# Performance work log

Measured on AMD Instinct MI355X. Metric: run time of the kernel, lower is better.

Reference implementation:

```python
import jax, jax.numpy as jnp
import numpy as np

SCALE_REACH = 10.0   # 'scale' in forward
SCALE_COS = 16.0     # CosNorm_Classifier default scale


def setup_inputs() -> dict:
    key = jax.random.key(0)
    ks = jax.random.split(key, 7)
    B, C, F = 64, 1000, 2048
    return {
        "x": jax.random.normal(ks[0], (B, F), jnp.float32),
        "centroids": jax.random.normal(ks[1], (C, F), jnp.float32),
        "W_hall": jax.random.normal(ks[2], (C, F), jnp.float32) * 0.02,
        "b_hall": jax.random.normal(ks[3], (C,), jnp.float32) * 0.02,
        "W_sel": jax.random.normal(ks[4], (F, F), jnp.float32) * 0.02,
        "b_sel": jax.random.normal(ks[5], (F,), jnp.float32) * 0.02,
        "W_cos": jax.random.normal(ks[6], (C, F), jnp.float32) * 0.001,
    }


def reference(x, centroids, W_hall, b_hall, W_sel, b_sel, W_cos):
    direct_feature = x
    # L2 distance to every class centroid: [B, C] (materializes [B, C, F] diff as in torch)
    diff = x[:, None, :] - centroids[None, :, :]
    dist = jnp.sqrt(jnp.sum(diff * diff, axis=2))
    # original sorts then takes column 0 -> min distance
    min_dist = jnp.min(dist, axis=1)                      # [B]
    reachability = (SCALE_REACH / min_dist)[:, None]      # [B, 1], broadcast over feat

    # hallucinated memory read
    values_memory = jax.nn.softmax(x @ W_hall.T + b_hall, axis=1)  # [B, C]
    memory_feature = values_memory @ centroids                      # [B, F]

    concept_selector = jnp.tanh(x @ W_sel.T + b_sel)                # [B, F]
    infused_feature = concept_selector * memory_feature
    feat = reachability * (direct_feature + infused_feature)

    # CosNorm classifier
    norm_x = jnp.linalg.norm(feat, axis=1, keepdims=True)           # [B, 1]
    ex = (norm_x / (1.0 + norm_x)) * (feat / norm_x)                # norm-gated unit vec
    ew = W_cos / jnp.linalg.norm(W_cos, axis=1, keepdims=True)      # [C, F]
    logits = ex @ (ew.T * SCALE_COS)                                # [B, C]

    return logits, direct_feature, infused_feature
```

## Files before the change

### kernel.cpp

```cpp
#include <hip/hip_runtime.h>
#include <math.h>

#define FF 2048

typedef __attribute__((ext_vector_type(8))) short short8;
typedef __attribute__((ext_vector_type(4))) float floatx4;

#define OFF_SPART 0
#define OFF_HPART 512000
#define OFF_SELP  1024000
#define OFF_MEMP  2072576
#define OFF_LOGP  3121152
#define OFF_V     3633152
#define OFF_FEAT  3697152
#define OFF_CN2   3828224
#define OFF_WINV  3829224
#define OFF_XN2   3830224
#define OFF_REACH 3830288
#define OFF_SFAC  3830352

#define TP 40

__device__ __forceinline__ void split2(float f, ushort& h, ushort& l) {
  unsigned u = __float_as_uint(f);
  float r = f - __uint_as_float(u & 0xffff0000u);
  h = (ushort)(u >> 16);
  l = (ushort)(__float_as_uint(r) >> 16);
}

__device__ __forceinline__ void stage_bt_bf(const float* __restrict__ M, int ldK, int rowBase,
                                            int nrows, int k0, int kmax,
                                            ushort* __restrict__ hi, ushort* __restrict__ lo, int t) {
  int r = t >> 2, q = t & 3;
  int grow = rowBase + r;
  bool rok = grow < nrows;
  const float* src = M + (size_t)grow * ldK + k0 + q * 8;
#pragma unroll
  for (int h = 0; h < 2; ++h) {
    int kb = k0 + q * 8 + h * 4;
    float4 v = make_float4(0.f, 0.f, 0.f, 0.f);
    if (rok) {
      if (kb + 3 < kmax) {
        v = *(const float4*)(src + h * 4);
      } else {
#pragma unroll
        for (int j = 0; j < 4; ++j)
          if (kb + j < kmax) ((float*)&v)[j] = src[h * 4 + j];
      }
    }
    ushort4 hv, lv;
    split2(v.x, hv.x, lv.x); split2(v.y, hv.y, lv.y);
    split2(v.z, hv.z, lv.z); split2(v.w, hv.w, lv.w);
    int base = r * TP + q * 8 + h * 4;
    *(ushort4*)(hi + base) = hv;
    *(ushort4*)(lo + base) = lv;
  }
}

__device__ __forceinline__ void stage_tr_bf(const float* __restrict__ M, int ldN, int k0, int kmax,
                                            int n0, ushort* __restrict__ hi, ushort* __restrict__ lo, int t) {
  int kk = t >> 3, c8 = (t & 7) * 8;
  int gk = k0 + kk;
  const float* src = M + (size_t)gk * ldN + n0 + c8;
  float4 v0 = make_float4(0.f, 0.f, 0.f, 0.f), v1 = v0;
  if (gk < kmax) { v0 = *(const float4*)src; v1 = *(const float4*)(src + 4); }
#pragma unroll
  for (int j = 0; j < 8; ++j) {
    float f = (j < 4) ? ((float*)&v0)[j] : ((float*)&v1)[j - 4];
    ushort h, l;
    split2(f, h, l);
    hi[(c8 + j) * TP + kk] = h;
    lo[(c8 + j) * TP + kk] = l;
  }
}

#define MFMA(a, b, c) __builtin_amdgcn_mfma_f32_16x16x32_bf16(a, b, c, 0, 0, 0)

__global__ __launch_bounds__(256) void k_phase1(
    const float* __restrict__ x, const float* __restrict__ cent,
    const float* __restrict__ whall, const float* __restrict__ wsel,
    const float* __restrict__ wcos, float* __restrict__ ws) {
  __shared__ ushort u_lds[6 * 64 * TP];
  ushort* Ah  = u_lds;
  ushort* Al  = u_lds + 64 * TP;
  ushort* B1h = u_lds + 2 * 64 * TP;
  ushort* B1l = u_lds + 3 * 64 * TP;
  ushort* B2h = u_lds + 4 * 64 * TP;
  ushort* B2l = u_lds + 5 * 64 * TP;
  int bx = blockIdx.x, t = threadIdx.x;
  int ln15 = t & 15;
  int lq = (t >> 4) & 3;
  int q8 = lq * 8;
  int w = t >> 6;
  int mh = w & 1, nh = w >> 1;

  if (bx < 128) {
    int tile = bx & 15, ks = bx >> 4;
    int n0 = tile * 64;
    floatx4 accS[2][2], accH[2][2];
#pragma unroll
    for (int i = 0; i < 2; ++i)
#pragma unroll
      for (int j = 0; j < 2; ++j) { accS[i][j] = (floatx4){0.f,0.f,0.f,0.f}; accH[i][j] = (floatx4){0.f,0.f,0.f,0.f}; }
    for (int kc = 0; kc < 8; ++kc) {
      int k0 = ks * 256 + kc * 32;
      __syncthreads();
      stage_bt_bf(x,     FF, 0,  64,   k0, FF, Ah,  Al,  t);
      stage_bt_bf(cent,  FF, n0, 1000, k0, FF, B1h, B1l, t);
      stage_bt_bf(whall, FF, n0, 1000, k0, FF, B2h, B2l, t);
      __syncthreads();
      short8 ah[2], al[2];
#pragma unroll
      for (int i = 0; i < 2; ++i) {
        int row = (mh * 2 + i) * 16 + ln15;
        ah[i] = *(const short8*)(Ah + row * TP + q8);
        al[i] = *(const short8*)(Al + row * TP + q8);
      }
#pragma unroll
      for (int j = 0; j < 2; ++j) {
        int brow = (nh * 2 + j) * 16 + ln15;
        short8 b1h = *(const short8*)(B1h + brow * TP + q8);
        short8 b1l = *(const short8*)(B1l + brow * TP + q8);
        short8 b2h = *(const short8*)(B2h + brow * TP + q8);
        short8 b2l = *(const short8*)(B2l + brow * TP + q8);
#pragma unroll
        for (int i = 0; i < 2; ++i) {
          accS[i][j] = MFMA(ah[i], b1h, accS[i][j]);
          accS[i][j] = MFMA(ah[i], b1l, accS[i][j]);
          accS[i][j] = MFMA(al[i], b1h, accS[i][j]);
          accH[i][j] = MFMA(ah[i], b2h, accH[i][j]);
          accH[i][j] = MFMA(ah[i], b2l, accH[i][j]);
          accH[i][j] = MFMA(al[i], b2h, accH[i][j]);
        }
      }
    }
    float* Spart = ws + OFF_SPART + (size_t)ks * 64000;
    float* Hpart = ws + OFF_HPART + (size_t)ks * 64000;
#pragma unroll
    for (int i = 0; i < 2; ++i)
#pragma unroll
      for (int j = 0; j < 2; ++j) {
        int gn = n0 + (nh * 2 + j) * 16 + ln15;
        if (gn < 1000) {
#pragma unroll
          for (int r = 0; r < 4; ++r) {
            int gm = (mh * 2 + i) * 16 + lq * 4 + r;
            Spart[gm * 1000 + gn] = accS[i][j][r];
            Hpart[gm * 1000 + gn] = accH[i][j][r];
          }
        }
      }
  } else if (bx < 384) {
    int b2 = bx - 128;
    int tile = b2 & 31, ks = b2 >> 5;
    int n0 = tile * 64;
    floatx4 acc[2][2];
#pragma unroll
    for (int i = 0; i < 2; ++i)
#pragma unroll
      for (int j = 0; j < 2; ++j) acc[i][j] = (floatx4){0.f,0.f,0.f,0.f};
    for (int kc = 0; kc < 8; ++kc) {
      int k0 = ks * 256 + kc * 32;
      __syncthreads();
      stage_bt_bf(x,    FF, 0,  64,  k0, FF, Ah,  Al,  t);
      stage_bt_bf(wsel, FF, n0, FF,  k0, FF, B1h, B1l, t);
      __syncthreads();
      short8 ah[2], al[2];
#pragma unroll
      for (int i = 0; i < 2; ++i) {
        int row = (mh * 2 + i) * 16 + ln15;
        ah[i] = *(const short8*)(Ah + row * TP + q8);
        al[i] = *(const short8*)(Al + row * TP + q8);
      }
#pragma unroll
      for (int j = 0; j < 2; ++j) {
        int brow = (nh * 2 + j) * 16 + ln15;
        short8 bh = *(const short8*)(B1h + brow * TP + q8);
        short8 bl = *(const short8*)(B1l + brow * TP + q8);
#pragma unroll
        for (int i = 0; i < 2; ++i) {
          acc[i][j] = MFMA(ah[i], bh, acc[i][j]);
          acc[i][j] = MFMA(ah[i], bl, acc[i][j]);
          acc[i][j] = MFMA(al[i], bh, acc[i][j]);
        }
      }
    }
    float* selp = ws + OFF_SELP + (size_t)ks * 131072;
#pragma unroll
    for (int i = 0; i < 2; ++i)
#pragma unroll
      for (int j = 0; j < 2; ++j) {
        int gn = n0 + (nh * 2 + j) * 16 + ln15;
#pragma unroll
        for (int r = 0; r < 4; ++r) {
          int gm = (mh * 2 + i) * 16 + lq * 4 + r;
          selp[gm * 2048 + gn] = acc[i][j][r];
        }
      }
  } else {
    int nb = bx - 384;
    int lane = t & 63;
    int r = nb * 4 + w;
    const float* src;
    if (r < 1000) src = cent + (size_t)r * FF;
    else if (r < 2000) src = wcos + (size_t)(r - 1000) * FF;
    else src = x + (size_t)(r - 2000) * FF;
    float s = 0.f;
#pragma unroll
    for (int i = 0; i < 8; ++i) {
      float4 v = *(const float4*)(src + i * 256 + lane * 4);
      s += v.x * v.x + v.y * v.y + v.z * v.z + v.w * v.w;
    }
#pragma unroll
    for (int off = 32; off > 0; off >>= 1) s += __shfl_down(s, off, 64);
    if (lane == 0) {
      if (r < 1000) ws[OFF_CN2 + r] = s;
      else if (r < 2000) ws[OFF_WINV + (r - 1000)] = 1.f / sqrtf(s);
      else ws[OFF_XN2 + (r - 2000)] = s;
    }
  }
}

__global__ __launch_bounds__(256) void k_softmax(const float* __restrict__ bhall,
                                                 float* __restrict__ ws) {
  int b = blockIdx.x, t = threadIdx.x;
  const float* Spart = ws + OFF_SPART;
  const float* Hpart = ws + OFF_HPART;
  __shared__ float hrow[1000];
  __shared__ float red[256];
  float xn = ws[OFF_XN2 + b];
  float lmin = 3.0e38f, lmax = -3.0e38f;
  for (int c = t; c < 1000; c += 256) {
    float S = 0.f, H = 0.f;
#pragma unroll
    for (int ks = 0; ks < 8; ++ks) {
      S += Spart[(size_t)ks * 64000 + b * 1000 + c];
      H += Hpart[(size_t)ks * 64000 + b * 1000 + c];
    }
    H += bhall[c];
    hrow[c] = H;
    float d2 = xn - 2.f * S + ws[OFF_CN2 + c];
    lmin = fminf(lmin, d2);
    lmax = fmaxf(lmax, H);
  }
  red[t] = lmin; __syncthreads();
  for (int s = 128; s > 0; s >>= 1) { if (t < s) red[t] = fminf(red[t], red[t + s]); __syncthreads(); }
  float bmin = red[0]; __syncthreads();
  red[t] = lmax; __syncthreads();
  for (int s = 128; s > 0; s >>= 1) { if (t < s) red[t] = fmaxf(red[t], red[t + s]); __syncthreads(); }
  float bmax = red[0]; __syncthreads();
  float lsum = 0.f;
  for (int c = t; c < 1000; c += 256) {
    float e = expf(hrow[c] - bmax);
    hrow[c] = e;
    lsum += e;
  }
  red[t] = lsum; __syncthreads();
  for (int s = 128; s > 0; s >>= 1) { if (t < s) red[t] += red[t + s]; __syncthreads(); }
  float inv = 1.f / red[0];
  float* V = ws + OFF_V;
  for (int c = t; c < 1000; c += 256) V[b * 1000 + c] = hrow[c] * inv;
  if (t == 0) ws[OFF_REACH + b] = 10.f / sqrtf(bmin);
}

__global__ __launch_bounds__(256) void k_mem(const float* __restrict__ cent,
                                             float* __restrict__ ws) {
  __shared__ ushort u_lds[4 * 64 * TP];
  ushort* Ah = u_lds;
  ushort* Al = u_lds + 64 * TP;
  ushort* Bh = u_lds + 2 * 64 * TP;
  ushort* Bl = u_lds + 3 * 64 * TP;
  int bx = blockIdx.x, t = threadIdx.x;
  int tile = bx & 31, ks = bx >> 5;
  int n0 = tile * 64;
  int ln15 = t & 15, lq = (t >> 4) & 3, q8 = lq * 8;
  int w = t >> 6, mh = w & 1, nh = w >> 1;
  const float* V = ws + OFF_V;
  floatx4 acc[2][2];
#pragma unroll
  for (int i = 0; i < 2; ++i)
#pragma unroll
    for (int j = 0; j < 2; ++j) acc[i][j] = (floatx4){0.f,0.f,0.f,0.f};
  for (int kc = 0; kc < 4; ++kc) {
    int k0 = ks * 128 + kc * 32;
    __syncthreads();
    stage_bt_bf(V, 1000, 0, 64, k0, 1000, Ah, Al, t);
    stage_tr_bf(cent, FF, k0, 1000, n0, Bh, Bl, t);
    __syncthreads();
    short8 ah[2], al[2];
#pragma unroll
    for (int i = 0; i < 2; ++i) {
      int row = (mh * 2 + i) * 16 + ln15;
      ah[i] = *(const short8*)(Ah + row * TP + q8);
      al[i] = *(const short8*)(Al + row * TP + q8);
    }
#pragma unroll
    for (int j = 0; j < 2; ++j) {
      int brow = (nh * 2 + j) * 16 + ln15;
      short8 bh = *(const short8*)(Bh + brow * TP + q8);
      short8 bl = *(const short8*)(Bl + brow * TP + q8);
#pragma unroll
      for (int i = 0; i < 2; ++i) {
        acc[i][j] = MFMA(ah[i], bh, acc[i][j]);
        acc[i][j] = MFMA(ah[i], bl, acc[i][j]);
        acc[i][j] = MFMA(al[i], bh, acc[i][j]);
      }
    }
  }
  float* memp = ws + OFF_MEMP + (size_t)ks * 131072;
#pragma unroll
  for (int i = 0; i < 2; ++i)
#pragma unroll
    for (int j = 0; j < 2; ++j) {
      int gn = n0 + (nh * 2 + j) * 16 + ln15;
#pragma unroll
      for (int r = 0; r < 4; ++r) {
        int gm = (mh * 2 + i) * 16 + lq * 4 + r;
        memp[gm * 2048 + gn] = acc[i][j][r];
      }
    }
}

__global__ __launch_bounds__(256) void k_fuse(const float* __restrict__ x,
                                              const float* __restrict__ bsel,
                                              float* __restrict__ ws, float* __restrict__ out) {
  int b = blockIdx.x, t = threadIdx.x;
  const float* selp = ws + OFF_SELP;
  const float* memp = ws + OFF_MEMP;
  float rch = ws[OFF_REACH + b];
  __shared__ float red[256];
  float nrm2 = 0.f;
  float* feat = ws + OFF_FEAT;
  for (int f = t; f < 2048; f += 256) {
    float sp = bsel[f], mm = 0.f;
#pragma unroll
    for (int ks = 0; ks < 8; ++ks) {
      sp += selp[(size_t)ks * 131072 + b * 2048 + f];
      mm += memp[(size_t)ks * 131072 + b * 2048 + f];
    }
    float sel = tanhf(sp);
    float inf = sel * mm;
    float xv = x[b * 2048 + f];
    float ft = rch * (xv + inf);
    out[64000 + b * 2048 + f] = xv;
    out[195072 + b * 2048 + f] = inf;
    feat[b * 2048 + f] = ft;
    nrm2 += ft * ft;
  }
  red[t] = nrm2; __syncthreads();
  for (int s = 128; s > 0; s >>= 1) { if (t < s) red[t] += red[t + s]; __syncthreads(); }
  if (t == 0) ws[OFF_SFAC + b] = 16.f / (1.f + sqrtf(red[0]));
}

__global__ __launch_bounds__(256) void k_loggemm(const float* __restrict__ wcos,
                                                 float* __restrict__ ws) {
  __shared__ ushort u_lds[4 * 64 * TP];
  ushort* Ah = u_lds;
  ushort* Al = u_lds + 64 * TP;
  ushort* Bh = u_lds + 2 * 64 * TP;
  ushort* Bl = u_lds + 3 * 64 * TP;
  int bx = blockIdx.x, t = threadIdx.x;
  int tile = bx & 15, ks = bx >> 4;
  int n0 = tile * 64;
  int ln15 = t & 15, lq = (t >> 4) & 3, q8 = lq * 8;
  int w = t >> 6, mh = w & 1, nh = w >> 1;
  const float* feat = ws + OFF_FEAT;
  floatx4 acc[2][2];
#pragma unroll
  for (int i = 0; i < 2; ++i)
#pragma unroll
    for (int j = 0; j < 2; ++j) acc[i][j] = (floatx4){0.f,0.f,0.f,0.f};
  for (int kc = 0; kc < 8; ++kc) {
    int k0 = ks * 256 + kc * 32;
    __syncthreads();
    stage_bt_bf(feat, FF, 0,  64,   k0, FF, Ah, Al, t);
    stage_bt_bf(wcos, FF, n0, 1000, k0, FF, Bh, Bl, t);
    __syncthreads();
    short8 ah[2], al[2];
#pragma unroll
    for (int i = 0; i < 2; ++i) {
      int row = (mh * 2 + i) * 16 + ln15;
      ah[i] = *(const short8*)(Ah + row * TP + q8);
      al[i] = *(const short8*)(Al + row * TP + q8);
    }
#pragma unroll
    for (int j = 0; j < 2; ++j) {
      int brow = (nh * 2 + j) * 16 + ln15;
      short8 bh = *(const short8*)(Bh + brow * TP + q8);
      short8 bl = *(const short8*)(Bl + brow * TP + q8);
#pragma unroll
      for (int i = 0; i < 2; ++i) {
        acc[i][j] = MFMA(ah[i], bh, acc[i][j]);
        acc[i][j] = MFMA(ah[i], bl, acc[i][j]);
        acc[i][j] = MFMA(al[i], bh, acc[i][j]);
      }
    }
  }
  float* logp = ws + OFF_LOGP + (size_t)ks * 64000;
#pragma unroll
  for (int i = 0; i < 2; ++i)
#pragma unroll
    for (int j = 0; j < 2; ++j) {
      int gn = n0 + (nh * 2 + j) * 16 + ln15;
      if (gn < 1000) {
#pragma unroll
        for (int r = 0; r < 4; ++r) {
          int gm = (mh * 2 + i) * 16 + lq * 4 + r;
          logp[gm * 1000 + gn] = acc[i][j][r];
        }
      }
    }
}

__global__ __launch_bounds__(256) void k_final(float* __restrict__ ws, float* __restrict__ out) {
  int idx = blockIdx.x * 256 + threadIdx.x;
  if (idx >= 64000) return;
  const float* logp = ws + OFF_LOGP;
  float s = 0.f;
#pragma unroll
  for (int ks = 0; ks < 8; ++ks) s += logp[(size_t)ks * 64000 + idx];
  int b = idx / 1000;
  int c = idx - b * 1000;
  out[idx] = s * ws[OFF_SFAC + b] * ws[OFF_WINV + c];
}

extern "C" void kernel_launch(void* const* d_in, const int* in_sizes, int n_in,
                              void* d_out, int out_size, void* d_ws, size_t ws_size,
                              hipStream_t stream) {
  const float* x     = (const float*)d_in[0];
  const float* cent  = (const float*)d_in[1];
  const float* whall = (const float*)d_in[2];
  const float* bhall = (const float*)d_in[3];
  const float* wsel  = (const float*)d_in[4];
  const float* bsel  = (const float*)d_in[5];
  const float* wcos  = (const float*)d_in[6];
  float* out = (float*)d_out;
  float* ws  = (float*)d_ws;

  hipLaunchKernelGGL(k_phase1, dim3(900), dim3(256), 0, stream, x, cent, whall, wsel, wcos, ws);
  hipLaunchKernelGGL(k_softmax, dim3(64), dim3(256), 0, stream, bhall, ws);
  hipLaunchKernelGGL(k_mem, dim3(256), dim3(256), 0, stream, cent, ws);
  hipLaunchKernelGGL(k_fuse, dim3(64), dim3(256), 0, stream, x, bsel, ws, out);
  hipLaunchKernelGGL(k_loggemm, dim3(128), dim3(256), 0, stream, wcos, ws);
  hipLaunchKernelGGL(k_final, dim3(250), dim3(256), 0, stream, ws, out);
}
```

Before: 144.4 us.

## Fuse all stages into one persistent kernel with atomic grid barriers

Replaces six kernel launches with a single 256-block kernel whose stages are separated by software grid barriers built on an atomic counter, plus a tiny init kernel that resets the counter. The work split changes as well: the W_sel GEMM now uses 128 blocks with larger K-chunks, the fuse step is spread across 256 blocks with partial norm sums, and the logits GEMM splits K 16 ways. The goal is to remove launch gaps and tail idle time between small dependent stages. In exchange it relies on all 256 blocks being resident at once, and every block pays spin-wait barrier latency at each stage boundary.

Measured after the change: 280.4 us. 94.1% more time.

```diff
diff --git a/kernel.cpp b/kernel.cpp
--- a/kernel.cpp
+++ b/kernel.cpp
@@ -9,15 +9,16 @@
 #define OFF_SPART 0
 #define OFF_HPART 512000
 #define OFF_SELP  1024000
-#define OFF_MEMP  2072576
-#define OFF_LOGP  3121152
-#define OFF_V     3633152
-#define OFF_FEAT  3697152
-#define OFF_CN2   3828224
-#define OFF_WINV  3829224
-#define OFF_XN2   3830224
-#define OFF_REACH 3830288
-#define OFF_SFAC  3830352
+#define OFF_MEMP  1548288
+#define OFF_LOGP  2596864
+#define OFF_V     3620864
+#define OFF_FEAT  3684864
+#define OFF_CN2   3815936
+#define OFF_WINV  3816936
+#define OFF_XN2   3817936
+#define OFF_REACH 3818000
+#define OFF_NRM2P 3818064
+#define OFF_BAR   3818320
 
 #define TP 40
 
@@ -76,23 +77,64 @@
 
 #define MFMA(a, b, c) __builtin_amdgcn_mfma_f32_16x16x32_bf16(a, b, c, 0, 0, 0)
 
-__global__ __launch_bounds__(256) void k_phase1(
+__device__ __forceinline__ void gbar(unsigned* __restrict__ bar, unsigned target) {
+  __syncthreads();
+  if (threadIdx.x == 0) {
+    __threadfence();
+    __hip_atomic_fetch_add(bar, 1u, __ATOMIC_RELEASE, __HIP_MEMORY_SCOPE_AGENT);
+    while (__hip_atomic_load(bar, __ATOMIC_ACQUIRE, __HIP_MEMORY_SCOPE_AGENT) < target)
+      __builtin_amdgcn_s_sleep(2);
+    __threadfence();
+  }
+  __syncthreads();
+}
+
+__global__ void k_init(unsigned* bar) {
+  if (threadIdx.x == 0)
+    __hip_atomic_store(bar, 0u, __ATOMIC_RELAXED, __HIP_MEMORY_SCOPE_AGENT);
+}
+
+#define NBLK 256
+
+__global__ __launch_bounds__(256) void k_all(
     const float* __restrict__ x, const float* __restrict__ cent,
-    const float* __restrict__ whall, const float* __restrict__ wsel,
-    const float* __restrict__ wcos, float* __restrict__ ws) {
-  __shared__ ushort u_lds[6 * 64 * TP];
-  ushort* Ah  = u_lds;
-  ushort* Al  = u_lds + 64 * TP;
-  ushort* B1h = u_lds + 2 * 64 * TP;
-  ushort* B1l = u_lds + 3 * 64 * TP;
-  ushort* B2h = u_lds + 4 * 64 * TP;
-  ushort* B2l = u_lds + 5 * 64 * TP;
+    const float* __restrict__ whall, const float* __restrict__ bhall,
+    const float* __restrict__ wsel, const float* __restrict__ bsel,
+    const float* __restrict__ wcos, float* __restrict__ ws, float* __restrict__ out) {
+  __shared__ __align__(16) char smem[6 * 64 * TP * 2];
+  ushort* Ah  = (ushort*)smem;
+  ushort* Al  = Ah + 64 * TP;
+  ushort* B1h = Ah + 2 * 64 * TP;
+  ushort* B1l = Ah + 3 * 64 * TP;
+  ushort* B2h = Ah + 4 * 64 * TP;
+  ushort* B2l = Ah + 5 * 64 * TP;
+  float* hrow = (float*)smem;
+  float* red  = (float*)smem + 1000;
+
   int bx = blockIdx.x, t = threadIdx.x;
-  int ln15 = t & 15;
-  int lq = (t >> 4) & 3;
-  int q8 = lq * 8;
-  int w = t >> 6;
+  int lane = t & 63, w = t >> 6;
+  int ln15 = t & 15, lq = (t >> 4) & 3, q8 = lq * 8;
   int mh = w & 1, nh = w >> 1;
+  unsigned* bar = (unsigned*)(ws + OFF_BAR);
+
+  for (int r = bx * 4 + w; r < 2064; r += 1024) {
+    const float* src = (r < 1000) ? cent + (size_t)r * FF
+                     : (r < 2000) ? wcos + (size_t)(r - 1000) * FF
+                                  : x + (size_t)(r - 2000) * FF;
+    float s = 0.f;
+#pragma unroll
+    for (int i = 0; i < 8; ++i) {
+      float4 v = *(const float4*)(src + i * 256 + lane * 4);
+      s += v.x * v.x + v.y * v.y + v.z * v.z + v.w * v.w;
+    }
+#pragma unroll
+    for (int off = 32; off > 0; off >>= 1) s += __shfl_down(s, off, 64);
+    if (lane == 0) {
+      if (r < 1000) ws[OFF_CN2 + r] = s;
+      else if (r < 2000) ws[OFF_WINV + (r - 1000)] = 1.f / sqrtf(s);
+      else ws[OFF_XN2 + (r - 2000)] = s;
+    }
+  }
 
   if (bx < 128) {
     int tile = bx & 15, ks = bx >> 4;
@@ -150,7 +192,7 @@
           }
         }
       }
-  } else if (bx < 384) {
+  } else {
     int b2 = bx - 128;
     int tile = b2 & 31, ks = b2 >> 5;
     int n0 = tile * 64;
@@ -159,11 +201,11 @@
     for (int i = 0; i < 2; ++i)
 #pragma unroll
       for (int j = 0; j < 2; ++j) acc[i][j] = (floatx4){0.f,0.f,0.f,0.f};
-    for (int kc = 0; kc < 8; ++kc) {
-      int k0 = ks * 256 + kc * 32;
-      __syncthreads();
-      stage_bt_bf(x,    FF, 0,  64,  k0, FF, Ah,  Al,  t);
-      stage_bt_bf(wsel, FF, n0, FF,  k0, FF, B1h, B1l, t);
+    for (int kc = 0; kc < 16; ++kc) {
+      int k0 = ks * 512 + kc * 32;
+      __syncthreads();
+      stage_bt_bf(x,    FF, 0,  64, k0, FF, Ah,  Al,  t);
+      stage_bt_bf(wsel, FF, n0, FF, k0, FF, B1h, B1l, t);
       __syncthreads();
       short8 ah[2], al[2];
 #pragma unroll
@@ -197,231 +239,203 @@
           selp[gm * 2048 + gn] = acc[i][j][r];
         }
       }
-  } else {
-    int nb = bx - 384;
-    int lane = t & 63;
-    int r = nb * 4 + w;
-    const float* src;
-    if (r < 1000) src = cent + (size_t)r * FF;
-    else if (r < 2000) src = wcos + (size_t)(r - 1000) * FF;
-    else src = x + (size_t)(r - 2000) * FF;
-    float s = 0.f;
-#pragma unroll
-    for (int i = 0; i < 8; ++i) {
-      float4 v = *(const float4*)(src + i * 256 + lane * 4);
-      s += v.x * v.x + v.y * v.y + v.z * v.z + v.w * v.w;
-    }
-#pragma unroll
-    for (int off = 32; off > 0; off >>= 1) s += __shfl_down(s, off, 64);
-    if (lane == 0) {
-      if (r < 1000) ws[OFF_CN2 + r] = s;
-      else if (r < 2000) ws[OFF_WINV + (r - 1000)] = 1.f / sqrtf(s);
-      else ws[OFF_XN2 + (r - 2000)] = s;
-    }
-  }
-}
-
-__global__ __launch_bounds__(256) void k_softmax(const float* __restrict__ bhall,
-                                                 float* __restrict__ ws) {
-  int b = blockIdx.x, t = threadIdx.x;
-  const float* Spart = ws + OFF_SPART;
-  const float* Hpart = ws + OFF_HPART;
-  __shared__ float hrow[1000];
-  __shared__ float red[256];
-  float xn = ws[OFF_XN2 + b];
-  float lmin = 3.0e38f, lmax = -3.0e38f;
-  for (int c = t; c < 1000; c += 256) {
-    float S = 0.f, H = 0.f;
-#pragma unroll
-    for (int ks = 0; ks < 8; ++ks) {
-      S += Spart[(size_t)ks * 64000 + b * 1000 + c];
-      H += Hpart[(size_t)ks * 64000 + b * 1000 + c];
-    }
-    H += bhall[c];
-    hrow[c] = H;
-    float d2 = xn - 2.f * S + ws[OFF_CN2 + c];
-    lmin = fminf(lmin, d2);
-    lmax = fmaxf(lmax, H);
-  }
-  red[t] = lmin; __syncthreads();
-  for (int s = 128; s > 0; s >>= 1) { if (t < s) red[t] = fminf(red[t], red[t + s]); __syncthreads(); }
-  float bmin = red[0]; __syncthreads();
-  red[t] = lmax; __syncthreads();
-  for (int s = 128; s > 0; s >>= 1) { if (t < s) red[t] = fmaxf(red[t], red[t + s]); __syncthreads(); }
-  float bmax = red[0]; __syncthreads();
-  float lsum = 0.f;
-  for (int c = t; c < 1000; c += 256) {
-    float e = expf(hrow[c] - bmax);
-    hrow[c] = e;
-    lsum += e;
-  }
-  red[t] = lsum; __syncthreads();
-  for (int s = 128; s > 0; s >>= 1) { if (t < s) red[t] += red[t + s]; __syncthreads(); }
-  float inv = 1.f / red[0];
-  float* V = ws + OFF_V;
-  for (int c = t; c < 1000; c += 256) V[b * 1000 + c] = hrow[c] * inv;
-  if (t == 0) ws[OFF_REACH + b] = 10.f / sqrtf(bmin);
-}
-
-__global__ __launch_bounds__(256) void k_mem(const float* __restrict__ cent,
-                                             float* __restrict__ ws) {
-  __shared__ ushort u_lds[4 * 64 * TP];
-  ushort* Ah = u_lds;
-  ushort* Al = u_lds + 64 * TP;
-  ushort* Bh = u_lds + 2 * 64 * TP;
-  ushort* Bl = u_lds + 3 * 64 * TP;
-  int bx = blockIdx.x, t = threadIdx.x;
-  int tile = bx & 31, ks = bx >> 5;
-  int n0 = tile * 64;
-  int ln15 = t & 15, lq = (t >> 4) & 3, q8 = lq * 8;
-  int w = t >> 6, mh = w & 1, nh = w >> 1;
-  const float* V = ws + OFF_V;
-  floatx4 acc[2][2];
-#pragma unroll
-  for (int i = 0; i < 2; ++i)
-#pragma unroll
-    for (int j = 0; j < 2; ++j) acc[i][j] = (floatx4){0.f,0.f,0.f,0.f};
-  for (int kc = 0; kc < 4; ++kc) {
-    int k0 = ks * 128 + kc * 32;
-    __syncthreads();
-    stage_bt_bf(V, 1000, 0, 64, k0, 1000, Ah, Al, t);
-    stage_tr_bf(cent, FF, k0, 1000, n0, Bh, Bl, t);
-    __syncthreads();
-    short8 ah[2], al[2];
-#pragma unroll
-    for (int i = 0; i < 2; ++i) {
-      int row = (mh * 2 + i) * 16 + ln15;
-      ah[i] = *(const short8*)(Ah + row * TP + q8);
-      al[i] = *(const short8*)(Al + row * TP + q8);
-    }
-#pragma unroll
-    for (int j = 0; j < 2; ++j) {
-      int brow = (nh * 2 + j) * 16 + ln15;
-      short8 bh = *(const short8*)(Bh + brow * TP + q8);
-      short8 bl = *(const short8*)(Bl + brow * TP + q8);
+  }
+
+  gbar(bar, NBLK);
+
+  if (bx < 64) {
+    int b = bx;
+    const float* Spart = ws + OFF_SPART;
+    const float* Hpart = ws + OFF_HPART;
+    float xn = ws[OFF_XN2 + b];
+    float lmin = 3.0e38f, lmax = -3.0e38f;
+    for (int c = t; c < 1000; c += 256) {
+      float S = 0.f, H = 0.f;
+#pragma unroll
+      for (int ks = 0; ks < 8; ++ks) {
+        S += Spart[(size_t)ks * 64000 + b * 1000 + c];
+        H += Hpart[(size_t)ks * 64000 + b * 1000 + c];
+      }
+      H += bhall[c];
+      hrow[c] = H;
+      float d2 = xn - 2.f * S + ws[OFF_CN2 + c];
+      lmin = fminf(lmin, d2);
+      lmax = fmaxf(lmax, H);
+    }
+    red[t] = lmin; __syncthreads();
+    for (int s = 128; s > 0; s >>= 1) { if (t < s) red[t] = fminf(red[t], red[t + s]); __syncthreads(); }
+    float bmin = red[0]; __syncthreads();
+    red[t] = lmax; __syncthreads();
+    for (int s = 128; s > 0; s >>= 1) { if (t < s) red[t] = fmaxf(red[t], red[t + s]); __syncthreads(); }
+    float bmax = red[0]; __syncthreads();
+    float lsum = 0.f;
+    for (int c = t; c < 1000; c += 256) {
+      float e = expf(hrow[c] - bmax);
+      hrow[c] = e;
+      lsum += e;
+    }
+    red[t] = lsum; __syncthreads();
+    for (int s = 128; s > 0; s >>= 1) { if (t < s) red[t] += red[t + s]; __syncthreads(); }
+    float inv = 1.f / red[0];
+    float* V = ws + OFF_V;
+    for (int c = t; c < 1000; c += 256) V[b * 1000 + c] = hrow[c] * inv;
+    if (t == 0) ws[OFF_REACH + b] = 10.f / sqrtf(bmin);
+  }
+
+  gbar(bar, 2 * NBLK);
+
+  {
+    int tile = bx & 31, ks = bx >> 5;
+    int n0 = tile * 64;
+    const float* V = ws + OFF_V;
+    floatx4 acc[2][2];
+#pragma unroll
+    for (int i = 0; i < 2; ++i)
+#pragma unroll
+      for (int j = 0; j < 2; ++j) acc[i][j] = (floatx4){0.f,0.f,0.f,0.f};
+    for (int kc = 0; kc < 4; ++kc) {
+      int k0 = ks * 128 + kc * 32;
+      __syncthreads();
+      stage_bt_bf(V, 1000, 0, 64, k0, 1000, Ah, Al, t);
+      stage_tr_bf(cent, FF, k0, 1000, n0, B1h, B1l, t);
+      __syncthreads();
+      short8 ah[2], al[2];
 #pragma unroll
       for (int i = 0; i < 2; ++i) {
-        acc[i][j] = MFMA(ah[i], bh, acc[i][j]);
-        acc[i][j] = MFMA(ah[i], bl, acc[i][j]);
-        acc[i][j] = MFMA(al[i], bh, acc[i][j]);
-      }
-    }
-  }
-  float* memp = ws + OFF_MEMP + (size_t)ks * 131072;
-#pragma unroll
-  for (int i = 0; i < 2; ++i)
-#pragma unroll
-    for (int j = 0; j < 2; ++j) {
-      int gn = n0 + (nh * 2 + j) * 16 + ln15;
-#pragma unroll
-      for (int r = 0; r < 4; ++r) {
-        int gm = (mh * 2 + i) * 16 + lq * 4 + r;
-        memp[gm * 2048 + gn] = acc[i][j][r];
-      }
-    }
-}
-
-__global__ __launch_bounds__(256) void k_fuse(const float* __restrict__ x,
-                                              const float* __restrict__ bsel,
-                                              float* __restrict__ ws, float* __restrict__ out) {
-  int b = blockIdx.x, t = threadIdx.x;
-  const float* selp = ws + OFF_SELP;
-  const float* memp = ws + OFF_MEMP;
-  float rch = ws[OFF_REACH + b];
-  __shared__ float red[256];
-  float nrm2 = 0.f;
-  float* feat = ws + OFF_FEAT;
-  for (int f = t; f < 2048; f += 256) {
-    float sp = bsel[f], mm = 0.f;
-#pragma unroll
-    for (int ks = 0; ks < 8; ++ks) {
-      sp += selp[(size_t)ks * 131072 + b * 2048 + f];
-      mm += memp[(size_t)ks * 131072 + b * 2048 + f];
-    }
-    float sel = tanhf(sp);
-    float inf = sel * mm;
-    float xv = x[b * 2048 + f];
-    float ft = rch * (xv + inf);
-    out[64000 + b * 2048 + f] = xv;
-    out[195072 + b * 2048 + f] = inf;
-    feat[b * 2048 + f] = ft;
-    nrm2 += ft * ft;
-  }
-  red[t] = nrm2; __syncthreads();
-  for (int s = 128; s > 0; s >>= 1) { if (t < s) red[t] += red[t + s]; __syncthreads(); }
-  if (t == 0) ws[OFF_SFAC + b] = 16.f / (1.f + sqrtf(red[0]));
-}
-
-__global__ __launch_bounds__(256) void k_loggemm(const float* __restrict__ wcos,
-                                                 float* __restrict__ ws) {
-  __shared__ ushort u_lds[4 * 64 * TP];
-  ushort* Ah = u_lds;
-  ushort* Al = u_lds + 64 * TP;
-  ushort* Bh = u_lds + 2 * 64 * TP;
-  ushort* Bl = u_lds + 3 * 64 * TP;
-  int bx = blockIdx.x, t = threadIdx.x;
-  int tile = bx & 15, ks = bx >> 4;
-  int n0 = tile * 64;
-  int ln15 = t & 15, lq = (t >> 4) & 3, q8 = lq * 8;
-  int w = t >> 6, mh = w & 1, nh = w >> 1;
-  const float* feat = ws + OFF_FEAT;
-  floatx4 acc[2][2];
-#pragma unroll
-  for (int i = 0; i < 2; ++i)
-#pragma unroll
-    for (int j = 0; j < 2; ++j) acc[i][j] = (floatx4){0.f,0.f,0.f,0.f};
-  for (int kc = 0; kc < 8; ++kc) {
-    int k0 = ks * 256 + kc * 32;
-    __syncthreads();
-    stage_bt_bf(feat, FF, 0,  64,   k0, FF, Ah, Al, t);
-    stage_bt_bf(wcos, FF, n0, 1000, k0, FF, Bh, Bl, t);
-    __syncthreads();
-    short8 ah[2], al[2];
-#pragma unroll
-    for (int i = 0; i < 2; ++i) {
-      int row = (mh * 2 + i) * 16 + ln15;
-      ah[i] = *(const short8*)(Ah + row * TP + q8);
-      al[i] = *(const short8*)(Al + row * TP + q8);
-    }
-#pragma unroll
-    for (int j = 0; j < 2; ++j) {
-      int brow = (nh * 2 + j) * 16 + ln15;
-      short8 bh = *(const short8*)(Bh + brow * TP + q8);
-      short8 bl = *(const short8*)(Bl + brow * TP + q8);
-#pragma unroll
-      for (int i = 0; i < 2; ++i) {
-        acc[i][j] = MFMA(ah[i], bh, acc[i][j]);
-        acc[i][j] = MFMA(ah[i], bl, acc[i][j]);
-        acc[i][j] = MFMA(al[i], bh, acc[i][j]);
-      }
-    }
-  }
-  float* logp = ws + OFF_LOGP + (size_t)ks * 64000;
-#pragma unroll
-  for (int i = 0; i < 2; ++i)
-#pragma unroll
-    for (int j = 0; j < 2; ++j) {
-      int gn = n0 + (nh * 2 + j) * 16 + ln15;
-      if (gn < 1000) {
+        int row = (mh * 2 + i) * 16 + ln15;
+        ah[i] = *(const short8*)(Ah + row * TP + q8);
+        al[i] = *(const short8*)(Al + row * TP + q8);
+      }
+#pragma unroll
+      for (int j = 0; j < 2; ++j) {
+        int brow = (nh * 2 + j) * 16 + ln15;
+        short8 bh = *(const short8*)(B1h + brow * TP + q8);
+        short8 bl = *(const short8*)(B1l + brow * TP + q8);
+#pragma unroll
+        for (int i = 0; i < 2; ++i) {
+          acc[i][j] = MFMA(ah[i], bh, acc[i][j]);
+          acc[i][j] = MFMA(ah[i], bl, acc[i][j]);
+          acc[i][j] = MFMA(al[i], bh, acc[i][j]);
+        }
+      }
+    }
+    float* memp = ws + OFF_MEMP + (size_t)ks * 131072;
+#pragma unroll
+    for (int i = 0; i < 2; ++i)
+#pragma unroll
+      for (int j = 0; j < 2; ++j) {
+        int gn = n0 + (nh * 2 + j) * 16 + ln15;
 #pragma unroll
         for (int r = 0; r < 4; ++r) {
           int gm = (mh * 2 + i) * 16 + lq * 4 + r;
-          logp[gm * 1000 + gn] = acc[i][j][r];
-        }
-      }
-    }
-}
-
-__global__ __launch_bounds__(256) void k_final(float* __restrict__ ws, float* __restrict__ out) {
-  int idx = blockIdx.x * 256 + threadIdx.x;
-  if (idx >= 64000) return;
-  const float* logp = ws + OFF_LOGP;
-  float s = 0.f;
-#pragma unroll
-  for (int ks = 0; ks < 8; ++ks) s += logp[(size_t)ks * 64000 + idx];
-  int b = idx / 1000;
-  int c = idx - b * 1000;
-  out[idx] = s * ws[OFF_SFAC + b] * ws[OFF_WINV + c];
+          memp[gm * 2048 + gn] = acc[i][j][r];
+        }
+      }
+  }
+
+  gbar(bar, 3 * NBLK);
+
+  {
+    int row = bx >> 2, chunk = bx & 3;
+    int f0 = chunk * 512;
+    const float* selp = ws + OFF_SELP;
+    const float* memp = ws + OFF_MEMP;
+    float* feat = ws + OFF_FEAT;
+    float rch = ws[OFF_REACH + row];
+    float nrm2 = 0.f;
+#pragma unroll
+    for (int ii = 0; ii < 2; ++ii) {
+      int f = f0 + ii * 256 + t;
+      float sp = bsel[f], mm = 0.f;
+#pragma unroll
+      for (int ks = 0; ks < 4; ++ks) sp += selp[(size_t)ks * 131072 + row * 2048 + f];
+#pragma unroll
+      for (int ks = 0; ks < 8; ++ks) mm += memp[(size_t)ks * 131072 + row * 2048 + f];
+      float sel = tanhf(sp);
+      float inf = sel * mm;
+      float xv = x[row * 2048 + f];
+      float ft = rch * (xv + inf);
+      out[64000 + row * 2048 + f] = xv;
+      out[195072 + row * 2048 + f] = inf;
+      feat[row * 2048 + f] = ft;
+      nrm2 += ft * ft;
+    }
+    __syncthreads();
+    red[t] = nrm2; __syncthreads();
+    for (int s = 128; s > 0; s >>= 1) { if (t < s) red[t] += red[t + s]; __syncthreads(); }
+    if (t == 0) ws[OFF_NRM2P + row * 4 + chunk] = red[0];
+  }
+
+  gbar(bar, 4 * NBLK);
+
+  {
+    int tile = bx & 15, ks = bx >> 4;
+    int n0 = tile * 64;
+    const float* feat = ws + OFF_FEAT;
+    floatx4 acc[2][2];
+#pragma unroll
+    for (int i = 0; i < 2; ++i)
+#pragma unroll
+      for (int j = 0; j < 2; ++j) acc[i][j] = (floatx4){0.f,0.f,0.f,0.f};
+    for (int kc = 0; kc < 4; ++kc) {
+      int k0 = ks * 128 + kc * 32;
+      __syncthreads();
+      stage_bt_bf(feat, FF, 0,  64,   k0, FF, Ah,  Al,  t);
+      stage_bt_bf(wcos, FF, n0, 1000, k0, FF, B1h, B1l, t);
+      __syncthreads();
+      short8 ah[2], al[2];
+#pragma unroll
+      for (int i = 0; i < 2; ++i) {
+        int row = (mh * 2 + i) * 16 + ln15;
+        ah[i] = *(const short8*)(Ah + row * TP + q8);
+        al[i] = *(const short8*)(Al + row * TP + q8);
+      }
+#pragma unroll
+      for (int j = 0; j < 2; ++j) {
+        int brow = (nh * 2 + j) * 16 + ln15;
+        short8 bh = *(const short8*)(B1h + brow * TP + q8);
+        short8 bl = *(const short8*)(B1l + brow * TP + q8);
+#pragma unroll
+        for (int i = 0; i < 2; ++i) {
+          acc[i][j] = MFMA(ah[i], bh, acc[i][j]);
+          acc[i][j] = MFMA(ah[i], bl, acc[i][j]);
+          acc[i][j] = MFMA(al[i], bh, acc[i][j]);
+        }
+      }
+    }
+    float* logp = ws + OFF_LOGP + (size_t)ks * 64000;
+#pragma unroll
+    for (int i = 0; i < 2; ++i)
+#pragma unroll
+      for (int j = 0; j < 2; ++j) {
+        int gn = n0 + (nh * 2 + j) * 16 + ln15;
+        if (gn < 1000) {
+#pragma unroll
+          for (int r = 0; r < 4; ++r) {
+            int gm = (mh * 2 + i) * 16 + lq * 4 + r;
+            logp[gm * 1000 + gn] = acc[i][j][r];
+          }
+        }
+      }
+  }
+
+  gbar(bar, 5 * NBLK);
+
+  {
+    int idx = bx * 250 + t;
+    if (t < 250) {
+      const float* logp = ws + OFF_LOGP;
+      float s = 0.f;
+#pragma unroll
+      for (int ks = 0; ks < 16; ++ks) s += logp[(size_t)ks * 64000 + idx];
+      int b = idx / 1000;
+      int c = idx - b * 1000;
+      float n2 = ws[OFF_NRM2P + b * 4 + 0] + ws[OFF_NRM2P + b * 4 + 1] +
+                 ws[OFF_NRM2P + b * 4 + 2] + ws[OFF_NRM2P + b * 4 + 3];
+      float sfac = 16.f / (1.f + sqrtf(n2));
+      out[idx] = s * sfac * ws[OFF_WINV + c];
+    }
+  }
 }
 
 extern "C" void kernel_launch(void* const* d_in, const int* in_sizes, int n_in,
@@ -436,11 +450,9 @@
   const float* wcos  = (const float*)d_in[6];
   float* out = (float*)d_out;
   float* ws  = (float*)d_ws;
-
-  hipLaunchKernelGGL(k_phase1, dim3(900), dim3(256), 0, stream, x, cent, whall, wsel, wcos, ws);
-  hipLaunchKernelGGL(k_softmax, dim3(64), dim3(256), 0, stream, bhall, ws);
-  hipLaunchKernelGGL(k_mem, dim3(256), dim3(256), 0, stream, cent, ws);
-  hipLaunchKernelGGL(k_fuse, dim3(64), dim3(256), 0, stream, x, bsel, ws, out);
-  hipLaunchKernelGGL(k_loggemm, dim3(128), dim3(256), 0, stream, wcos, ws);
-  hipLaunchKernelGGL(k_final, dim3(250), dim3(256), 0, stream, ws, out);
-}
+  unsigned* bar = (unsigned*)(ws + OFF_BAR);
+
+  hipLaunchKernelGGL(k_init, dim3(1), dim3(64), 0, stream, bar);
+  hipLaunchKernelGGL(k_all, dim3(NBLK), dim3(256), 0, stream,
+                     x, cent, whall, bhall, wsel, bsel, wcos, ws, out);
+}
```

## Fold row norms into GEMM blocks, vectorize reductions, widen fuse and logits split-K

Applied to the files above, without the earlier changes.

Row-norm computation moves from dedicated extra blocks into a grid-stride prologue inside the 512 GEMM blocks, so the first launch shrinks from 900 blocks. Softmax and the fuse kernel switch to float4 vectorized partial-sum loads. The fuse kernel spreads each row over 8 blocks of 64 threads and writes partial norms, with the final scaling moved into the last kernel. The logits GEMM doubles its split-K to 16 slices to raise block count, and V gets padded to a 1024 stride for aligned vector staging. In exchange there are more partial buffers to sum and redundant norm reads in the final kernel.

Result: faster. 133.5 us, median of 2 (-7.5%).

```diff
diff --git a/kernel.cpp b/kernel.cpp
--- a/kernel.cpp
+++ b/kernel.cpp
@@ -11,13 +11,13 @@
 #define OFF_SELP  1024000
 #define OFF_MEMP  2072576
 #define OFF_LOGP  3121152
-#define OFF_V     3633152
-#define OFF_FEAT  3697152
-#define OFF_CN2   3828224
-#define OFF_WINV  3829224
-#define OFF_XN2   3830224
-#define OFF_REACH 3830288
-#define OFF_SFAC  3830352
+#define OFF_V     4145152
+#define OFF_FEAT  4210688
+#define OFF_CN2   4341760
+#define OFF_WINV  4342760
+#define OFF_XN2   4343760
+#define OFF_REACH 4343824
+#define OFF_NRM2P 4343888
 
 #define TP 40
 
@@ -76,11 +76,11 @@
 
 #define MFMA(a, b, c) __builtin_amdgcn_mfma_f32_16x16x32_bf16(a, b, c, 0, 0, 0)
 
-__global__ __launch_bounds__(256) void k_phase1(
+__global__ __launch_bounds__(256) void ka_gemm1(
     const float* __restrict__ x, const float* __restrict__ cent,
     const float* __restrict__ whall, const float* __restrict__ wsel,
     const float* __restrict__ wcos, float* __restrict__ ws) {
-  __shared__ ushort u_lds[6 * 64 * TP];
+  __shared__ __align__(16) ushort u_lds[6 * 64 * TP];
   ushort* Ah  = u_lds;
   ushort* Al  = u_lds + 64 * TP;
   ushort* B1h = u_lds + 2 * 64 * TP;
@@ -88,11 +88,28 @@
   ushort* B2h = u_lds + 4 * 64 * TP;
   ushort* B2l = u_lds + 5 * 64 * TP;
   int bx = blockIdx.x, t = threadIdx.x;
-  int ln15 = t & 15;
-  int lq = (t >> 4) & 3;
-  int q8 = lq * 8;
-  int w = t >> 6;
+  int lane = t & 63, w = t >> 6;
+  int ln15 = t & 15, lq = (t >> 4) & 3, q8 = lq * 8;
   int mh = w & 1, nh = w >> 1;
+
+  for (int r = bx * 4 + w; r < 2064; r += 2048) {
+    const float* src = (r < 1000) ? cent + (size_t)r * FF
+                     : (r < 2000) ? wcos + (size_t)(r - 1000) * FF
+                                  : x + (size_t)(r - 2000) * FF;
+    float s = 0.f;
+#pragma unroll
+    for (int i = 0; i < 8; ++i) {
+      float4 v = *(const float4*)(src + i * 256 + lane * 4);
+      s += v.x * v.x + v.y * v.y + v.z * v.z + v.w * v.w;
+    }
+#pragma unroll
+    for (int off = 32; off > 0; off >>= 1) s += __shfl_down(s, off, 64);
+    if (lane == 0) {
+      if (r < 1000) ws[OFF_CN2 + r] = s;
+      else if (r < 2000) ws[OFF_WINV + (r - 1000)] = 1.f / sqrtf(s);
+      else ws[OFF_XN2 + (r - 2000)] = s;
+    }
+  }
 
   if (bx < 128) {
     int tile = bx & 15, ks = bx >> 4;
@@ -162,8 +179,8 @@
     for (int kc = 0; kc < 8; ++kc) {
       int k0 = ks * 256 + kc * 32;
       __syncthreads();
-      stage_bt_bf(x,    FF, 0,  64,  k0, FF, Ah,  Al,  t);
-      stage_bt_bf(wsel, FF, n0, FF,  k0, FF, B1h, B1l, t);
+      stage_bt_bf(x,    FF, 0,  64, k0, FF, Ah,  Al,  t);
+      stage_bt_bf(wsel, FF, n0, FF, k0, FF, B1h, B1l, t);
       __syncthreads();
       short8 ah[2], al[2];
 #pragma unroll
@@ -197,51 +214,35 @@
           selp[gm * 2048 + gn] = acc[i][j][r];
         }
       }
-  } else {
-    int nb = bx - 384;
-    int lane = t & 63;
-    int r = nb * 4 + w;
-    const float* src;
-    if (r < 1000) src = cent + (size_t)r * FF;
-    else if (r < 2000) src = wcos + (size_t)(r - 1000) * FF;
-    else src = x + (size_t)(r - 2000) * FF;
-    float s = 0.f;
-#pragma unroll
-    for (int i = 0; i < 8; ++i) {
-      float4 v = *(const float4*)(src + i * 256 + lane * 4);
-      s += v.x * v.x + v.y * v.y + v.z * v.z + v.w * v.w;
-    }
-#pragma unroll
-    for (int off = 32; off > 0; off >>= 1) s += __shfl_down(s, off, 64);
-    if (lane == 0) {
-      if (r < 1000) ws[OFF_CN2 + r] = s;
-      else if (r < 2000) ws[OFF_WINV + (r - 1000)] = 1.f / sqrtf(s);
-      else ws[OFF_XN2 + (r - 2000)] = s;
-    }
-  }
-}
-
-__global__ __launch_bounds__(256) void k_softmax(const float* __restrict__ bhall,
-                                                 float* __restrict__ ws) {
-  int b = blockIdx.x, t = threadIdx.x;
-  const float* Spart = ws + OFF_SPART;
-  const float* Hpart = ws + OFF_HPART;
+  }
+}
+
+__global__ __launch_bounds__(256) void kb_softmax(const float* __restrict__ bhall,
+                                                  float* __restrict__ ws) {
   __shared__ float hrow[1000];
   __shared__ float red[256];
+  int b = blockIdx.x, t = threadIdx.x;
   float xn = ws[OFF_XN2 + b];
   float lmin = 3.0e38f, lmax = -3.0e38f;
-  for (int c = t; c < 1000; c += 256) {
-    float S = 0.f, H = 0.f;
+  if (t < 250) {
+    int c0 = t * 4;
+    floatx4 S = {0.f,0.f,0.f,0.f}, H = {0.f,0.f,0.f,0.f};
 #pragma unroll
     for (int ks = 0; ks < 8; ++ks) {
-      S += Spart[(size_t)ks * 64000 + b * 1000 + c];
-      H += Hpart[(size_t)ks * 64000 + b * 1000 + c];
-    }
-    H += bhall[c];
-    hrow[c] = H;
-    float d2 = xn - 2.f * S + ws[OFF_CN2 + c];
-    lmin = fminf(lmin, d2);
-    lmax = fmaxf(lmax, H);
+      floatx4 sv = *(const floatx4*)(ws + OFF_SPART + (size_t)ks * 64000 + b * 1000 + c0);
+      floatx4 hv = *(const floatx4*)(ws + OFF_HPART + (size_t)ks * 64000 + b * 1000 + c0);
+      S += sv; H += hv;
+    }
+    floatx4 bh = *(const floatx4*)(bhall + c0);
+    floatx4 cn = *(const floatx4*)(ws + OFF_CN2 + c0);
+#pragma unroll
+    for (int j = 0; j < 4; ++j) {
+      float Hf = H[j] + bh[j];
+      hrow[c0 + j] = Hf;
+      float d2 = xn - 2.f * S[j] + cn[j];
+      lmin = fminf(lmin, d2);
+      lmax = fmaxf(lmax, Hf);
+    }
   }
   red[t] = lmin; __syncthreads();
   for (int s = 128; s > 0; s >>= 1) { if (t < s) red[t] = fminf(red[t], red[t + s]); __syncthreads(); }
@@ -250,26 +251,34 @@
   for (int s = 128; s > 0; s >>= 1) { if (t < s) red[t] = fmaxf(red[t], red[t + s]); __syncthreads(); }
   float bmax = red[0]; __syncthreads();
   float lsum = 0.f;
-  for (int c = t; c < 1000; c += 256) {
-    float e = expf(hrow[c] - bmax);
-    hrow[c] = e;
-    lsum += e;
+  float e4[4] = {0.f, 0.f, 0.f, 0.f};
+  if (t < 250) {
+#pragma unroll
+    for (int j = 0; j < 4; ++j) {
+      e4[j] = expf(hrow[t * 4 + j] - bmax);
+      lsum += e4[j];
+    }
   }
   red[t] = lsum; __syncthreads();
   for (int s = 128; s > 0; s >>= 1) { if (t < s) red[t] += red[t + s]; __syncthreads(); }
   float inv = 1.f / red[0];
-  float* V = ws + OFF_V;
-  for (int c = t; c < 1000; c += 256) V[b * 1000 + c] = hrow[c] * inv;
+  if (t < 250)
+    *(floatx4*)(ws + OFF_V + b * 1024 + t * 4) =
+        (floatx4){e4[0] * inv, e4[1] * inv, e4[2] * inv, e4[3] * inv};
+  if (t == 250) {
+#pragma unroll
+    for (int j = 0; j < 24; ++j) ws[OFF_V + b * 1024 + 1000 + j] = 0.f;
+  }
   if (t == 0) ws[OFF_REACH + b] = 10.f / sqrtf(bmin);
 }
 
-__global__ __launch_bounds__(256) void k_mem(const float* __restrict__ cent,
-                                             float* __restrict__ ws) {
-  __shared__ ushort u_lds[4 * 64 * TP];
-  ushort* Ah = u_lds;
-  ushort* Al = u_lds + 64 * TP;
-  ushort* Bh = u_lds + 2 * 64 * TP;
-  ushort* Bl = u_lds + 3 * 64 * TP;
+__global__ __launch_bounds__(256) void kc_mem(const float* __restrict__ cent,
+                                              float* __restrict__ ws) {
+  __shared__ __align__(16) ushort u_lds[4 * 64 * TP];
+  ushort* Ah  = u_lds;
+  ushort* Al  = u_lds + 64 * TP;
+  ushort* B1h = u_lds + 2 * 64 * TP;
+  ushort* B1l = u_lds + 3 * 64 * TP;
   int bx = blockIdx.x, t = threadIdx.x;
   int tile = bx & 31, ks = bx >> 5;
   int n0 = tile * 64;
@@ -284,8 +293,20 @@
   for (int kc = 0; kc < 4; ++kc) {
     int k0 = ks * 128 + kc * 32;
     __syncthreads();
-    stage_bt_bf(V, 1000, 0, 64, k0, 1000, Ah, Al, t);
-    stage_tr_bf(cent, FF, k0, 1000, n0, Bh, Bl, t);
+    {
+      int r = t >> 2, q = t & 3;
+#pragma unroll
+      for (int h = 0; h < 2; ++h) {
+        float4 v = *(const float4*)(V + (size_t)r * 1024 + k0 + q * 8 + h * 4);
+        ushort4 hv, lv;
+        split2(v.x, hv.x, lv.x); split2(v.y, hv.y, lv.y);
+        split2(v.z, hv.z, lv.z); split2(v.w, hv.w, lv.w);
+        int base = r * TP + q * 8 + h * 4;
+        *(ushort4*)(Ah + base) = hv;
+        *(ushort4*)(Al + base) = lv;
+      }
+    }
+    stage_tr_bf(cent, FF, k0, 1000, n0, B1h, B1l, t);
     __syncthreads();
     short8 ah[2], al[2];
 #pragma unroll
@@ -297,8 +318,8 @@
 #pragma unroll
     for (int j = 0; j < 2; ++j) {
       int brow = (nh * 2 + j) * 16 + ln15;
-      short8 bh = *(const short8*)(Bh + brow * TP + q8);
-      short8 bl = *(const short8*)(Bl + brow * TP + q8);
+      short8 bh = *(const short8*)(B1h + brow * TP + q8);
+      short8 bl = *(const short8*)(B1l + brow * TP + q8);
 #pragma unroll
       for (int i = 0; i < 2; ++i) {
         acc[i][j] = MFMA(ah[i], bh, acc[i][j]);
@@ -321,44 +342,50 @@
     }
 }
 
-__global__ __launch_bounds__(256) void k_fuse(const float* __restrict__ x,
+__global__ __launch_bounds__(64) void kd_fuse(const float* __restrict__ x,
                                               const float* __restrict__ bsel,
                                               float* __restrict__ ws, float* __restrict__ out) {
-  int b = blockIdx.x, t = threadIdx.x;
-  const float* selp = ws + OFF_SELP;
-  const float* memp = ws + OFF_MEMP;
-  float rch = ws[OFF_REACH + b];
-  __shared__ float red[256];
+  int bx = blockIdx.x, t = threadIdx.x;
+  int row = bx >> 3, ch = bx & 7;
+  int f = ch * 256 + t * 4;
+  const float* selp = ws + OFF_SELP + (size_t)row * 2048 + f;
+  const float* memp = ws + OFF_MEMP + (size_t)row * 2048 + f;
+  floatx4 sp = {0.f,0.f,0.f,0.f}, mm = {0.f,0.f,0.f,0.f};
+#pragma unroll
+  for (int ks = 0; ks < 8; ++ks) {
+    sp += *(const floatx4*)(selp + (size_t)ks * 131072);
+    mm += *(const floatx4*)(memp + (size_t)ks * 131072);
+  }
+  float4 bs4 = *(const float4*)(bsel + f);
+  float4 x4  = *(const float4*)(x + (size_t)row * 2048 + f);
+  float rch = ws[OFF_REACH + row];
+  float4 inf4;
+  floatx4 ft4;
   float nrm2 = 0.f;
-  float* feat = ws + OFF_FEAT;
-  for (int f = t; f < 2048; f += 256) {
-    float sp = bsel[f], mm = 0.f;
-#pragma unroll
-    for (int ks = 0; ks < 8; ++ks) {
-      sp += selp[(size_t)ks * 131072 + b * 2048 + f];
-      mm += memp[(size_t)ks * 131072 + b * 2048 + f];
-    }
-    float sel = tanhf(sp);
-    float inf = sel * mm;
-    float xv = x[b * 2048 + f];
-    float ft = rch * (xv + inf);
-    out[64000 + b * 2048 + f] = xv;
-    out[195072 + b * 2048 + f] = inf;
-    feat[b * 2048 + f] = ft;
+#pragma unroll
+  for (int j = 0; j < 4; ++j) {
+    float sel = tanhf(sp[j] + ((float*)&bs4)[j]);
+    float inf = sel * mm[j];
+    float ft = rch * (((float*)&x4)[j] + inf);
+    ((float*)&inf4)[j] = inf;
+    ft4[j] = ft;
     nrm2 += ft * ft;
   }
-  red[t] = nrm2; __syncthreads();
-  for (int s = 128; s > 0; s >>= 1) { if (t < s) red[t] += red[t + s]; __syncthreads(); }
-  if (t == 0) ws[OFF_SFAC + b] = 16.f / (1.f + sqrtf(red[0]));
-}
-
-__global__ __launch_bounds__(256) void k_loggemm(const float* __restrict__ wcos,
+  *(float4*)(out + 64000 + (size_t)row * 2048 + f) = x4;
+  *(float4*)(out + 195072 + (size_t)row * 2048 + f) = inf4;
+  *(floatx4*)(ws + OFF_FEAT + (size_t)row * 2048 + f) = ft4;
+#pragma unroll
+  for (int off = 32; off > 0; off >>= 1) nrm2 += __shfl_down(nrm2, off, 64);
+  if (t == 0) ws[OFF_NRM2P + row * 8 + ch] = nrm2;
+}
+
+__global__ __launch_bounds__(256) void ke_logits(const float* __restrict__ wcos,
                                                  float* __restrict__ ws) {
-  __shared__ ushort u_lds[4 * 64 * TP];
-  ushort* Ah = u_lds;
-  ushort* Al = u_lds + 64 * TP;
-  ushort* Bh = u_lds + 2 * 64 * TP;
-  ushort* Bl = u_lds + 3 * 64 * TP;
+  __shared__ __align__(16) ushort u_lds[4 * 64 * TP];
+  ushort* Ah  = u_lds;
+  ushort* Al  = u_lds + 64 * TP;
+  ushort* B1h = u_lds + 2 * 64 * TP;
+  ushort* B1l = u_lds + 3 * 64 * TP;
   int bx = blockIdx.x, t = threadIdx.x;
   int tile = bx & 15, ks = bx >> 4;
   int n0 = tile * 64;
@@ -370,11 +397,23 @@
   for (int i = 0; i < 2; ++i)
 #pragma unroll
     for (int j = 0; j < 2; ++j) acc[i][j] = (floatx4){0.f,0.f,0.f,0.f};
-  for (int kc = 0; kc < 8; ++kc) {
-    int k0 = ks * 256 + kc * 32;
+  for (int kc = 0; kc < 4; ++kc) {
+    int k0 = ks * 128 + kc * 32;
     __syncthreads();
-    stage_bt_bf(feat, FF, 0,  64,   k0, FF, Ah, Al, t);
-    stage_bt_bf(wcos, FF, n0, 1000, k0, FF, Bh, Bl, t);
+    {
+      int r = t >> 2, q = t & 3;
+#pragma unroll
+      for (int h = 0; h < 2; ++h) {
+        float4 v = *(const float4*)(feat + (size_t)r * 2048 + k0 + q * 8 + h * 4);
+        ushort4 hv, lv;
+        split2(v.x, hv.x, lv.x); split2(v.y, hv.y, lv.y);
+        split2(v.z, hv.z, lv.z); split2(v.w, hv.w, lv.w);
+        int base = r * TP + q * 8 + h * 4;
+        *(ushort4*)(Ah + base) = hv;
+        *(ushort4*)(Al + base) = lv;
+      }
+    }
+    stage_bt_bf(wcos, FF, n0, 1000, k0, FF, B1h, B1l, t);
     __syncthreads();
     short8 ah[2], al[2];
 #pragma unroll
@@ -386,8 +425,8 @@
 #pragma unroll
     for (int j = 0; j < 2; ++j) {
       int brow = (nh * 2 + j) * 16 + ln15;
-      short8 bh = *(const short8*)(Bh + brow * TP + q8);
-      short8 bl = *(const short8*)(Bl + brow * TP + q8);
+      short8 bh = *(const short8*)(B1h + brow * TP + q8);
+      short8 bl = *(const short8*)(B1l + brow * TP + q8);
 #pragma unroll
       for (int i = 0; i < 2; ++i) {
         acc[i][j] = MFMA(ah[i], bh, acc[i][j]);
@@ -412,16 +451,32 @@
     }
 }
 
-__global__ __launch_bounds__(256) void k_final(float* __restrict__ ws, float* __restrict__ out) {
-  int idx = blockIdx.x * 256 + threadIdx.x;
-  if (idx >= 64000) return;
-  const float* logp = ws + OFF_LOGP;
-  float s = 0.f;
-#pragma unroll
-  for (int ks = 0; ks < 8; ++ks) s += logp[(size_t)ks * 64000 + idx];
-  int b = idx / 1000;
-  int c = idx - b * 1000;
-  out[idx] = s * ws[OFF_SFAC + b] * ws[OFF_WINV + c];
+__global__ __launch_bounds__(128) void kf_final(float* __restrict__ ws, float* __restrict__ out) {
+  int bx = blockIdx.x, t = threadIdx.x;
+  int idx0 = (bx * 128 + t) * 4;
+  const float* logp = ws + OFF_LOGP + idx0;
+  floatx4 s = {0.f,0.f,0.f,0.f};
+#pragma unroll
+  for (int ks = 0; ks < 16; ++ks)
+    s += *(const floatx4*)(logp + (size_t)ks * 64000);
+  floatx4 o4;
+  int pb = -1;
+  float sfac = 0.f;
+#pragma unroll
+  for (int j = 0; j < 4; ++j) {
+    int idx = idx0 + j;
+    int bb = idx / 1000;
+    int cc = idx - bb * 1000;
+    if (bb != pb) {
+      float n2 = 0.f;
+#pragma unroll
+      for (int q = 0; q < 8; ++q) n2 += ws[OFF_NRM2P + bb * 8 + q];
+      sfac = 16.f / (1.f + sqrtf(n2));
+      pb = bb;
+    }
+    o4[j] = s[j] * sfac * ws[OFF_WINV + cc];
+  }
+  *(floatx4*)(out + idx0) = o4;
 }
 
 extern "C" void kernel_launch(void* const* d_in, const int* in_sizes, int n_in,
@@ -437,10 +492,10 @@
   float* out = (float*)d_out;
   float* ws  = (float*)d_ws;
 
-  hipLaunchKernelGGL(k_phase1, dim3(900), dim3(256), 0, stream, x, cent, whall, wsel, wcos, ws);
-  hipLaunchKernelGGL(k_softmax, dim3(64), dim3(256), 0, stream, bhall, ws);
-  hipLaunchKernelGGL(k_mem, dim3(256), dim3(256), 0, stream, cent, ws);
-  hipLaunchKernelGGL(k_fuse, dim3(64), dim3(256), 0, stream, x, bsel, ws, out);
-  hipLaunchKernelGGL(k_loggemm, dim3(128), dim3(256), 0, stream, wcos, ws);
-  hipLaunchKernelGGL(k_final, dim3(250), dim3(256), 0, stream, ws, out);
-}
+  hipLaunchKernelGGL(ka_gemm1,   dim3(512), dim3(256), 0, stream, x, cent, whall, wsel, wcos, ws);
+  hipLaunchKernelGGL(kb_softmax, dim3(64),  dim3(256), 0, stream, bhall, ws);
+  hipLaunchKernelGGL(kc_mem,     dim3(256), dim3(256), 0, stream, cent, ws);
+  hipLaunchKernelGGL(kd_fuse,    dim3(512), dim3(64),  0, stream, x, bsel, ws, out);
+  hipLaunchKernelGGL(ke_logits,  dim3(256), dim3(256), 0, stream, wcos, ws);
+  hipLaunchKernelGGL(kf_final,   dim3(125), dim3(128), 0, stream, ws, out);
+}
```
